# Kernel optimization log

Hardware: AMD Instinct MI355X
Metric: run time of the kernel (lower is better)

## Reference

```python
import jax, jax.numpy as jnp
import numpy as np

NUM_HEADS = 8
NUM_KV_HEADS = 2
HEAD_DIM = 64
EPS = 1e-6
ROPE_BASE = 10000.0


def rmsnorm(x, w):
    # x: (..., head_dim)
    var = jnp.mean(x * x, axis=-1, keepdims=True)
    return x * jax.lax.rsqrt(var + EPS) * w


def apply_rope(x):
    # x: (B, L, nH, hd); positions along L, standard rotate-half RoPE
    B, L, nH, hd = x.shape
    inv_freq = 1.0 / (ROPE_BASE ** (jnp.arange(0, hd, 2, dtype=jnp.float32) / hd))  # (hd/2,)
    ang = jnp.arange(L, dtype=jnp.float32)[:, None] * inv_freq[None, :]  # (L, hd/2)
    cos = jnp.concatenate([jnp.cos(ang), jnp.cos(ang)], axis=-1)[None, :, None, :]  # (1,L,1,hd)
    sin = jnp.concatenate([jnp.sin(ang), jnp.sin(ang)], axis=-1)[None, :, None, :]
    x1, x2 = jnp.split(x, 2, axis=-1)
    rot = jnp.concatenate([-x2, x1], axis=-1)
    return x * cos + rot * sin


def setup_inputs() -> dict:
    key = jax.random.key(0)
    ks = jax.random.split(key, 6)
    width = 512
    x = jax.random.normal(ks[0], (1, 16, 16, 16, width), dtype=jnp.float32)
    s = 1.0 / np.sqrt(width)
    Wq = jax.random.normal(ks[1], (width, width), dtype=jnp.float32) * s
    Wk = jax.random.normal(ks[2], (NUM_KV_HEADS * HEAD_DIM, width), dtype=jnp.float32) * s
    Wv = jax.random.normal(ks[3], (NUM_KV_HEADS * HEAD_DIM, width), dtype=jnp.float32) * s
    Wo = jax.random.normal(ks[4], (width, width), dtype=jnp.float32) * s
    q_norm_w = jnp.ones((HEAD_DIM,), dtype=jnp.float32)
    k_norm_w = jnp.ones((HEAD_DIM,), dtype=jnp.float32)
    return {"x": x, "Wq": Wq, "Wk": Wk, "Wv": Wv,
            "q_norm_w": q_norm_w, "k_norm_w": k_norm_w, "Wo": Wo}


def reference(x, Wq, Wk, Wv, q_norm_w, k_norm_w, Wo):
    B, H, W, D, C = x.shape
    L = H * W * D
    xf = x.reshape(B, L, C)
    q = (xf @ Wq.T).reshape(B, L, NUM_HEADS, HEAD_DIM)
    k = (xf @ Wk.T).reshape(B, L, NUM_KV_HEADS, HEAD_DIM)
    v = (xf @ Wv.T).reshape(B, L, NUM_KV_HEADS, HEAD_DIM)
    q = apply_rope(rmsnorm(q, q_norm_w))
    k = apply_rope(rmsnorm(k, k_norm_w))
    # (B, heads, L, hd)
    q = q.transpose(0, 2, 1, 3)
    k = k.transpose(0, 2, 1, 3)
    v = v.transpose(0, 2, 1, 3)
    repeats = NUM_HEADS // NUM_KV_HEADS
    if repeats > 1:
        k = jnp.repeat(k, repeats, axis=1)
        v = jnp.repeat(v, repeats, axis=1)
    scale = 1.0 / np.sqrt(HEAD_DIM)
    scores = jnp.einsum('bhqd,bhkd->bhqk', q, k) * scale
    attn = jax.nn.softmax(scores, axis=-1)
    out = jnp.einsum('bhqk,bhkd->bhqd', attn, v)
    out = out.transpose(0, 2, 1, 3).reshape(B, H, W, D, C)
    return out @ Wo.T
```

## Files before the change

### kernel.cpp

```cpp
#include <hip/hip_runtime.h>
#include <hip/hip_bf16.h>
#include <math.h>

#define L_SEQ 4096
#define CDIM  512
#define NH    8
#define NKV   2
#define HD    64
#define EPS   1e-6f
#define QSCALE 0.18033688011f

using short8 = __attribute__((ext_vector_type(8))) short;
using f32x4  = __attribute__((ext_vector_type(4))) float;
using f32x16 = __attribute__((ext_vector_type(16))) float;
typedef unsigned short ushort_t;

__device__ __forceinline__ ushort_t f2bf(float f) {
    union { float f; unsigned u; } c; c.f = f;
    unsigned r = c.u + 0x7FFF + ((c.u >> 16) & 1);
    return (ushort_t)(r >> 16);
}
__device__ __forceinline__ float bf2f(ushort_t u) {
    union { unsigned u; float f; } c; c.u = ((unsigned)u) << 16;
    return c.f;
}

#define GLOAD_LDS16(g, l)                                                  \
    __builtin_amdgcn_global_load_lds(                                      \
        (const __attribute__((address_space(1))) unsigned int*)(g),        \
        (__attribute__((address_space(3))) unsigned int*)(l), 16, 0, 0)

__device__ __forceinline__ short8 lds_read8(const char* p) {
    return *reinterpret_cast<const short8*>(__builtin_assume_aligned(p, 16));
}

__device__ __forceinline__ unsigned pk_bf16(float lo, float hi) {
    const __hip_bfloat162 h2 = __float22bfloat162_rn(make_float2(lo, hi));
    unsigned w; __builtin_memcpy(&w, &h2, 4);
    return w;
}

__global__ __launch_bounds__(256) void cvt_bf16(const float* __restrict__ x,
                                                const float* __restrict__ wq,
                                                const float* __restrict__ wk,
                                                const float* __restrict__ wv,
                                                const float* __restrict__ wo,
                                                ushort_t* __restrict__ xb,
                                                ushort_t* __restrict__ wqb,
                                                ushort_t* __restrict__ wkb,
                                                ushort_t* __restrict__ wvb,
                                                ushort_t* __restrict__ wob) {
    const size_t i = ((size_t)blockIdx.x * 256 + threadIdx.x) << 2;
    const float* s; ushort_t* d; size_t o;
    if (i < 2097152)      { s = x;  d = xb;  o = i; }
    else if (i < 2359296) { s = wq; d = wqb; o = i - 2097152; }
    else if (i < 2424832) { s = wk; d = wkb; o = i - 2359296; }
    else if (i < 2490368) { s = wv; d = wvb; o = i - 2424832; }
    else                  { s = wo; d = wob; o = i - 2490368; }
    const float4 v = *reinterpret_cast<const float4*>(s + o);
    ushort_t r[4] = { f2bf(v.x), f2bf(v.y), f2bf(v.z), f2bf(v.w) };
    *reinterpret_cast<uint2*>(d + o) = *reinterpret_cast<const uint2*>(r);
}

template<bool OUT_BF16>
__global__ __launch_bounds__(256) void gemm_bf16_nt(const ushort_t* __restrict__ A,
                                                    const ushort_t* __restrict__ B,
                                                    void* __restrict__ Cv,
                                                    int M, int N, int K) {
    __shared__ short As[2][4096];
    __shared__ short Bs[2][4096];

    const int tid = threadIdx.x;
    const int w = tid >> 6, lane = tid & 63;
    const int g = lane >> 4, r16 = lane & 15;
    const int wr = w >> 1, wc = w & 1;
    const int m0 = blockIdx.y * 64, n0 = blockIdx.x * 64;
    const int r7sw = (r16 & 7) << 4;

    const int lrow = lane >> 3;
    const int swzb = ((lane & 7) ^ lrow) << 4;
    const int c0 = w * 2, c1 = w * 2 + 1;
    const size_t rowK2 = (size_t)K * 2;

    const char* agA = (const char*)A + (size_t)(m0 + c0 * 8 + lrow) * rowK2 + swzb;
    const char* agB = agA + 8 * rowK2;
    const char* bgA = (const char*)B + (size_t)(n0 + c0 * 8 + lrow) * rowK2 + swzb;
    const char* bgB = bgA + 8 * rowK2;

    GLOAD_LDS16(agA, (char*)As[0] + c0 * 1024);
    GLOAD_LDS16(agB, (char*)As[0] + c1 * 1024);
    GLOAD_LDS16(bgA, (char*)Bs[0] + c0 * 1024);
    GLOAD_LDS16(bgB, (char*)Bs[0] + c1 * 1024);
    __syncthreads();

    f32x4 acc[2][2] = {};
    const int NKIT = K >> 6;
    int cur = 0;
    for (int it = 0; it < NKIT; ++it) {
        if (it + 1 < NKIT) {
            const size_t ko = (size_t)(it + 1) * 128;
            char* ad = (char*)As[cur ^ 1];
            char* bd = (char*)Bs[cur ^ 1];
            GLOAD_LDS16(agA + ko, ad + c0 * 1024);
            GLOAD_LDS16(agB + ko, ad + c1 * 1024);
            GLOAD_LDS16(bgA + ko, bd + c0 * 1024);
            GLOAD_LDS16(bgB + ko, bd + c1 * 1024);
        }
        const char* at = (const char*)As[cur];
        const char* bt = (const char*)Bs[cur];

        short8 af[2][2], bfr[2][2];
#pragma unroll
        for (int t = 0; t < 2; ++t)
#pragma unroll
            for (int ks = 0; ks < 2; ++ks) {
                af[t][ks]  = lds_read8(at + (wr * 32 + t * 16 + r16) * 128
                                          + ((ks * 64 + g * 16) ^ r7sw));
                bfr[t][ks] = lds_read8(bt + (wc * 32 + t * 16 + r16) * 128
                                          + ((ks * 64 + g * 16) ^ r7sw));
            }
        __builtin_amdgcn_s_setprio(1);
#pragma unroll
        for (int tm = 0; tm < 2; ++tm)
#pragma unroll
            for (int tn = 0; tn < 2; ++tn)
#pragma unroll
                for (int ks = 0; ks < 2; ++ks)
                    acc[tm][tn] = __builtin_amdgcn_mfma_f32_16x16x32_bf16(
                        af[tm][ks], bfr[tn][ks], acc[tm][tn], 0, 0, 0);
        __builtin_amdgcn_s_setprio(0);

        __syncthreads();
        cur ^= 1;
    }

#pragma unroll
    for (int tm = 0; tm < 2; ++tm)
#pragma unroll
        for (int tn = 0; tn < 2; ++tn)
#pragma unroll
            for (int jj = 0; jj < 4; ++jj) {
                const int row = m0 + wr * 32 + tm * 16 + g * 4 + jj;
                const int col = n0 + wc * 32 + tn * 16 + r16;
                if (OUT_BF16)
                    ((ushort_t*)Cv)[(size_t)row * N + col] = f2bf(acc[tm][tn][jj]);
                else
                    ((float*)Cv)[(size_t)row * N + col] = acc[tm][tn][jj];
            }
}

__global__ __launch_bounds__(256) void norm_rope(ushort_t* __restrict__ q,
                                                 ushort_t* __restrict__ k,
                                                 const float* __restrict__ qw,
                                                 const float* __restrict__ kw) {
    const int wid  = threadIdx.x >> 6;
    const int lane = threadIdx.x & 63;
    const long row = (long)blockIdx.x * 4 + wid;
    const long QROWS = (long)L_SEQ * NH;

    ushort_t* ptr;
    const float* w;
    int pos;
    const bool isq = (row < QROWS);
    if (isq) {
        pos = (int)(row >> 3);
        ptr = q + (size_t)pos * (NH * HD) + (int)(row & 7) * HD;
        w = qw;
    } else {
        const long r = row - QROWS;
        pos = (int)(r >> 1);
        ptr = k + (size_t)pos * (NKV * HD) + (int)(r & 1) * HD;
        w = kw;
    }

    float x = bf2f(ptr[lane]);
    float ss = x * x;
#pragma unroll
    for (int off = 32; off; off >>= 1) ss += __shfl_xor(ss, off);
    float xn = x * rsqrtf(ss * (1.0f / 64.0f) + EPS) * w[lane];

    float xp = __shfl_xor(xn, 32);
    const int i = lane & 31;
    const float inv_freq = exp2f((float)i * -0.41524101186f);
    float s, c;
    sincosf((float)pos * inv_freq, &s, &c);
    float out = (lane < 32) ? (xn * c - xp * s) : (xn * c + xp * s);
    if (isq) out *= QSCALE;
    ptr[lane] = f2bf(out);
}

__global__ __launch_bounds__(256, 2) void attn_mfma(const ushort_t* __restrict__ qb,
                                                    const ushort_t* __restrict__ kb,
                                                    const ushort_t* __restrict__ vtb,
                                                    ushort_t* __restrict__ opart,
                                                    float* __restrict__ lpart) {
    __shared__ short Ks[2][4096];
    __shared__ short Vs[2][4096];

    const int tid = threadIdx.x;
    const int w = tid >> 6, lane = tid & 63;
    const int l31 = lane & 31, hf = lane >> 5;
    const int h = blockIdx.y, hkv = h >> 2;
    const int s = blockIdx.z;
    const int kvspan = L_SEQ / gridDim.z;
    const int kvb = s * kvspan;
    const int qw = blockIdx.x * 256 + w * 64;
    const int swz = (lane & 7) << 4;

    const int lrow = lane >> 3;
    const int swzb = ((lane & 7) ^ lrow) << 4;
    const int c0 = w * 2, c1 = w * 2 + 1;

    const char* kgA = (const char*)kb + (size_t)(kvb + c0 * 8 + lrow) * (NKV * HD * 2)
                      + hkv * (HD * 2) + swzb;
    const char* kgB = kgA + 8 * (NKV * HD * 2);
    const char* vgA = (const char*)vtb + (size_t)(hkv * HD + c0 * 8 + lrow) * (L_SEQ * 2)
                      + (size_t)kvb * 2 + swzb;
    const char* vgB = vgA + 8 * (size_t)(L_SEQ * 2);

    short8 qf0[4], qf1[4];
#pragma unroll
    for (int ks = 0; ks < 4; ++ks) {
        qf0[ks] = *reinterpret_cast<const short8*>(
            &qb[(size_t)(qw + l31) * CDIM + h * HD + ks * 16 + hf * 8]);
        qf1[ks] = *reinterpret_cast<const short8*>(
            &qb[(size_t)(qw + 32 + l31) * CDIM + h * HD + ks * 16 + hf * 8]);
    }

    GLOAD_LDS16(kgA, (char*)Ks[0] + c0 * 1024);
    GLOAD_LDS16(kgB, (char*)Ks[0] + c1 * 1024);
    GLOAD_LDS16(vgA, (char*)Vs[0] + c0 * 1024);
    GLOAD_LDS16(vgB, (char*)Vs[0] + c1 * 1024);
    __syncthreads();

    f32x16 oacc0[2] = {}, oacc1[2] = {};
    float ls0[2] = {}, ls1[2] = {};

    int cur = 0;
    const int nit = kvspan >> 6;
    for (int it = 0; it < nit; ++it) {
        if (it + 1 < nit) {
            const size_t ko = (size_t)(it + 1) * 64 * (NKV * HD * 2);
            const size_t vo = (size_t)(it + 1) * 128;
            char* kd = (char*)Ks[cur ^ 1];
            char* vd = (char*)Vs[cur ^ 1];
            GLOAD_LDS16(kgA + ko, kd + c0 * 1024);
            GLOAD_LDS16(kgB + ko, kd + c1 * 1024);
            GLOAD_LDS16(vgA + vo, vd + c0 * 1024);
            GLOAD_LDS16(vgB + vo, vd + c1 * 1024);
        }

        const char* kt = (const char*)Ks[cur];
        const char* vt = (const char*)Vs[cur];

#pragma unroll
        for (int sub = 0; sub < 2; ++sub) {
            f32x16 s0 = {}, s1 = {};
            __builtin_amdgcn_s_setprio(1);
#pragma unroll
            for (int ks = 0; ks < 4; ++ks) {
                const short8 kfr = lds_read8(
                    kt + (sub * 32 + l31) * 128 + ((ks * 32 + hf * 16) ^ swz));
                s0 = __builtin_amdgcn_mfma_f32_32x32x16_bf16(kfr, qf0[ks], s0, 0, 0, 0);
                s1 = __builtin_amdgcn_mfma_f32_32x32x16_bf16(kfr, qf1[ks], s1, 0, 0, 0);
            }
            __builtin_amdgcn_s_setprio(0);

            unsigned pk0[8], pk1[8];
#pragma unroll
            for (int r2 = 0; r2 < 8; ++r2) {
                const float x0 = exp2f(s0[2 * r2]), y0 = exp2f(s0[2 * r2 + 1]);
                const float x1 = exp2f(s1[2 * r2]), y1 = exp2f(s1[2 * r2 + 1]);
                ls0[r2 & 1] += x0 + y0;
                ls1[r2 & 1] += x1 + y1;
                pk0[r2] = pk_bf16(x0, y0);
                pk1[r2] = pk_bf16(x1, y1);
            }

            short8 pf0[2], pf1[2];
#pragma unroll
            for (int kkl = 0; kkl < 2; ++kkl) {
                auto a0 = __builtin_amdgcn_permlane32_swap(pk0[kkl * 4 + 0], pk0[kkl * 4 + 2], false, false);
                auto a1 = __builtin_amdgcn_permlane32_swap(pk0[kkl * 4 + 1], pk0[kkl * 4 + 3], false, false);
                auto b0 = __builtin_amdgcn_permlane32_swap(pk1[kkl * 4 + 0], pk1[kkl * 4 + 2], false, false);
                auto b1 = __builtin_amdgcn_permlane32_swap(pk1[kkl * 4 + 1], pk1[kkl * 4 + 3], false, false);
                union { unsigned u[4]; short8 s8; } u0, u1;
                u0.u[0] = a0[0]; u0.u[1] = a1[0]; u0.u[2] = a0[1]; u0.u[3] = a1[1];
                u1.u[0] = b0[0]; u1.u[1] = b1[0]; u1.u[2] = b0[1]; u1.u[3] = b1[1];
                pf0[kkl] = u0.s8; pf1[kkl] = u1.s8;
            }

            __builtin_amdgcn_s_setprio(1);
#pragma unroll
            for (int n = 0; n < 2; ++n) {
#pragma unroll
                for (int kkl = 0; kkl < 2; ++kkl) {
                    const short8 vf = lds_read8(
                        vt + (n * 32 + l31) * 128 + (((sub * 2 + kkl) * 32 + hf * 16) ^ swz));
                    oacc0[n] = __builtin_amdgcn_mfma_f32_32x32x16_bf16(pf0[kkl], vf, oacc0[n], 0, 0, 0);
                    oacc1[n] = __builtin_amdgcn_mfma_f32_32x32x16_bf16(pf1[kkl], vf, oacc1[n], 0, 0, 0);
                }
            }
            __builtin_amdgcn_s_setprio(0);
        }

        __syncthreads();
        cur ^= 1;
    }

    float lsA = ls0[0] + ls0[1];
    float lsB = ls1[0] + ls1[1];
    lsA += __shfl_xor(lsA, 32);
    lsB += __shfl_xor(lsB, 32);
    ushort_t* op = opart + (size_t)s * L_SEQ * CDIM;
    float* lp = lpart + (size_t)s * L_SEQ * NH;
    if (lane < 32) {
        lp[(size_t)(qw + lane) * NH + h] = lsA;
        lp[(size_t)(qw + 32 + lane) * NH + h] = lsB;
    }
#pragma unroll
    for (int n = 0; n < 2; ++n)
#pragma unroll
        for (int r = 0; r < 16; ++r) {
            const int rr = (r & 3) + 8 * (r >> 2) + 4 * hf;
            op[(size_t)(qw + rr) * CDIM + h * HD + n * 32 + l31] = f2bf(oacc0[n][r]);
            op[(size_t)(qw + 32 + rr) * CDIM + h * HD + n * 32 + l31] = f2bf(oacc1[n][r]);
        }
}

__global__ __launch_bounds__(256) void combine_splits(const ushort_t* __restrict__ opart,
                                                      const float* __restrict__ lpart,
                                                      ushort_t* __restrict__ out,
                                                      int nsplit) {
    const size_t i4 = ((size_t)blockIdx.x * 256 + threadIdx.x) << 2;
    const int row = (int)(i4 >> 9);
    const int h = (int)((i4 & 511) >> 6);
    float l = 0.0f;
    for (int s = 0; s < nsplit; ++s)
        l += lpart[(size_t)s * L_SEQ * NH + (size_t)row * NH + h];
    const float inv = 1.0f / l;

    float acc[4] = {};
    for (int s = 0; s < nsplit; ++s) {
        ushort_t a[4];
        *reinterpret_cast<uint2*>(a) =
            *reinterpret_cast<const uint2*>(opart + (size_t)s * L_SEQ * CDIM + i4);
#pragma unroll
        for (int j = 0; j < 4; ++j) acc[j] += bf2f(a[j]);
    }
    ushort_t r[4];
#pragma unroll
    for (int j = 0; j < 4; ++j) r[j] = f2bf(acc[j] * inv);
    *reinterpret_cast<uint2*>(out + i4) = *reinterpret_cast<const uint2*>(r);
}

extern "C" void kernel_launch(void* const* d_in, const int* in_sizes, int n_in,
                              void* d_out, int out_size, void* d_ws, size_t ws_size,
                              hipStream_t stream) {
    const float* x   = (const float*)d_in[0];
    const float* Wq  = (const float*)d_in[1];
    const float* Wk  = (const float*)d_in[2];
    const float* Wv  = (const float*)d_in[3];
    const float* qnw = (const float*)d_in[4];
    const float* knw = (const float*)d_in[5];
    const float* Wo  = (const float*)d_in[6];
    float* out = (float*)d_out;

    const size_t tail = (size_t)L_SEQ * CDIM * 2
                      + (size_t)L_SEQ * NKV * HD * 2 * 2
                      + (size_t)CDIM * CDIM * 2 * 2
                      + (size_t)NKV * HD * CDIM * 2 * 2
                      + (size_t)8 * L_SEQ * NH * 4;
    const size_t need8 = (size_t)8 * L_SEQ * CDIM * 2 + tail;
    const int nsplit = (ws_size >= need8) ? 8 : 4;

    char* p = (char*)d_ws;
    ushort_t* opart = (ushort_t*)p;
    ushort_t* xb    = opart;
    ushort_t* abuf  = opart;
    char* q = p + (size_t)nsplit * L_SEQ * CDIM * 2;
    ushort_t* qbuf = (ushort_t*)q;
    ushort_t* kbuf = qbuf + (size_t)L_SEQ * CDIM;
    ushort_t* vtb  = kbuf + (size_t)L_SEQ * NKV * HD;
    ushort_t* wqb  = vtb  + (size_t)L_SEQ * NKV * HD;
    ushort_t* wkb  = wqb  + (size_t)CDIM * CDIM;
    ushort_t* wvb  = wkb  + (size_t)NKV * HD * CDIM;
    ushort_t* wob  = wvb  + (size_t)NKV * HD * CDIM;
    float*    lpart = (float*)(wob + (size_t)CDIM * CDIM);

    const dim3 blk(256);

    cvt_bf16<<<dim3(2688), blk, 0, stream>>>(x, Wq, Wk, Wv, Wo, xb, wqb, wkb, wvb, wob);

    gemm_bf16_nt<true><<<dim3(8, 64),  blk, 0, stream>>>(xb, wqb, qbuf, L_SEQ, CDIM, CDIM);
    gemm_bf16_nt<true><<<dim3(2, 64),  blk, 0, stream>>>(xb, wkb, kbuf, L_SEQ, NKV * HD, CDIM);
    gemm_bf16_nt<true><<<dim3(64, 2),  blk, 0, stream>>>(wvb, xb, vtb, NKV * HD, L_SEQ, CDIM);

    norm_rope<<<dim3((L_SEQ * (NH + NKV)) / 4), blk, 0, stream>>>(qbuf, kbuf, qnw, knw);

    attn_mfma<<<dim3(L_SEQ / 256, NH, nsplit), blk, 0, stream>>>(qbuf, kbuf, vtb, opart, lpart);

    combine_splits<<<dim3((L_SEQ * CDIM) / (256 * 4)), blk, 0, stream>>>(opart, lpart, abuf, nsplit);

    gemm_bf16_nt<false><<<dim3(8, 64), blk, 0, stream>>>(abuf, wob, out, L_SEQ, CDIM, CDIM);
}
```

Measured before the change: 115.1 us.

## Fuse Q/K/V projections and RMSNorm+RoPE into one GEMM kernel

Replaces three separate projection GEMM launches and the standalone norm_rope kernel with a single qkv_gemm kernel. Block IDs are partitioned across the Q, K and transposed V products. For Q and K tiles, the accumulator is staged through shared memory so RMSNorm, RoPE and the Q scale are applied before the bf16 store. This removes three launches and a full read-modify-write pass over Q and K in global memory, at the cost of an extra LDS staging pass and serial per-row epilogue work inside each GEMM block.

New measurement: 102.5 us. -11.0%, faster.

```diff
diff --git a/kernel.cpp b/kernel.cpp
--- a/kernel.cpp
+++ b/kernel.cpp
@@ -62,6 +62,135 @@
     *reinterpret_cast<uint2*>(d + o) = *reinterpret_cast<const uint2*>(r);
 }
 
+__global__ __launch_bounds__(256) void qkv_gemm(const ushort_t* __restrict__ xb,
+                                                const ushort_t* __restrict__ wqb,
+                                                const ushort_t* __restrict__ wkb,
+                                                const ushort_t* __restrict__ wvb,
+                                                const float* __restrict__ qnw,
+                                                const float* __restrict__ knw,
+                                                ushort_t* __restrict__ qbuf,
+                                                ushort_t* __restrict__ kbuf,
+                                                ushort_t* __restrict__ vtb) {
+    __shared__ char smem[32768];
+    short (*As)[4096] = (short(*)[4096])smem;
+    short (*Bs)[4096] = (short(*)[4096])(smem + 16384);
+    float (*F)[65]    = (float(*)[65])smem;
+
+    const int bid = blockIdx.x;
+    int which, m0, n0;
+    const ushort_t *A, *B;
+    if (bid < 512)      { which = 0; A = xb;  B = wqb; m0 = (bid >> 3) * 64; n0 = (bid & 7) * 64; }
+    else if (bid < 640) { which = 1; A = xb;  B = wkb; const int i = bid - 512; m0 = (i >> 1) * 64; n0 = (i & 1) * 64; }
+    else                { which = 2; A = wvb; B = xb;  const int i = bid - 640; m0 = (i & 1) * 64; n0 = (i >> 1) * 64; }
+
+    const int tid = threadIdx.x;
+    const int w = tid >> 6, lane = tid & 63;
+    const int g = lane >> 4, r16 = lane & 15;
+    const int wr = w >> 1, wc = w & 1;
+    const int r7sw = (r16 & 7) << 4;
+
+    const int lrow = lane >> 3;
+    const int swzb = ((lane & 7) ^ lrow) << 4;
+    const int c0 = w * 2, c1 = w * 2 + 1;
+    const size_t rowK2 = (size_t)CDIM * 2;
+
+    const char* agA = (const char*)A + (size_t)(m0 + c0 * 8 + lrow) * rowK2 + swzb;
+    const char* agB = agA + 8 * rowK2;
+    const char* bgA = (const char*)B + (size_t)(n0 + c0 * 8 + lrow) * rowK2 + swzb;
+    const char* bgB = bgA + 8 * rowK2;
+
+    GLOAD_LDS16(agA, (char*)As[0] + c0 * 1024);
+    GLOAD_LDS16(agB, (char*)As[0] + c1 * 1024);
+    GLOAD_LDS16(bgA, (char*)Bs[0] + c0 * 1024);
+    GLOAD_LDS16(bgB, (char*)Bs[0] + c1 * 1024);
+    __syncthreads();
+
+    f32x4 acc[2][2] = {};
+    int cur = 0;
+    for (int it = 0; it < CDIM / 64; ++it) {
+        if (it + 1 < CDIM / 64) {
+            const size_t ko = (size_t)(it + 1) * 128;
+            char* ad = (char*)As[cur ^ 1];
+            char* bd = (char*)Bs[cur ^ 1];
+            GLOAD_LDS16(agA + ko, ad + c0 * 1024);
+            GLOAD_LDS16(agB + ko, ad + c1 * 1024);
+            GLOAD_LDS16(bgA + ko, bd + c0 * 1024);
+            GLOAD_LDS16(bgB + ko, bd + c1 * 1024);
+        }
+        const char* at = (const char*)As[cur];
+        const char* bt = (const char*)Bs[cur];
+
+        short8 af[2][2], bfr[2][2];
+#pragma unroll
+        for (int t = 0; t < 2; ++t)
+#pragma unroll
+            for (int ks = 0; ks < 2; ++ks) {
+                af[t][ks]  = lds_read8(at + (wr * 32 + t * 16 + r16) * 128
+                                          + ((ks * 64 + g * 16) ^ r7sw));
+                bfr[t][ks] = lds_read8(bt + (wc * 32 + t * 16 + r16) * 128
+                                          + ((ks * 64 + g * 16) ^ r7sw));
+            }
+        __builtin_amdgcn_s_setprio(1);
+#pragma unroll
+        for (int tm = 0; tm < 2; ++tm)
+#pragma unroll
+            for (int tn = 0; tn < 2; ++tn)
+#pragma unroll
+                for (int ks = 0; ks < 2; ++ks)
+                    acc[tm][tn] = __builtin_amdgcn_mfma_f32_16x16x32_bf16(
+                        af[tm][ks], bfr[tn][ks], acc[tm][tn], 0, 0, 0);
+        __builtin_amdgcn_s_setprio(0);
+
+        __syncthreads();
+        cur ^= 1;
+    }
+
+    if (which == 2) {
+#pragma unroll
+        for (int tm = 0; tm < 2; ++tm)
+#pragma unroll
+            for (int tn = 0; tn < 2; ++tn)
+#pragma unroll
+                for (int jj = 0; jj < 4; ++jj) {
+                    const int row = m0 + wr * 32 + tm * 16 + g * 4 + jj;
+                    const int col = n0 + wc * 32 + tn * 16 + r16;
+                    vtb[(size_t)row * L_SEQ + col] = f2bf(acc[tm][tn][jj]);
+                }
+        return;
+    }
+
+#pragma unroll
+    for (int tm = 0; tm < 2; ++tm)
+#pragma unroll
+        for (int tn = 0; tn < 2; ++tn)
+#pragma unroll
+            for (int jj = 0; jj < 4; ++jj)
+                F[wr * 32 + tm * 16 + g * 4 + jj][wc * 32 + tn * 16 + r16] = acc[tm][tn][jj];
+    __syncthreads();
+
+    const float wv_ = (which == 0 ? qnw : knw)[lane];
+    const int i31 = lane & 31;
+    const float invf = exp2f((float)i31 * -0.41524101186f);
+    ushort_t* dst = (which == 0) ? qbuf : kbuf;
+    const int ncols = (which == 0) ? (NH * HD) : (NKV * HD);
+
+    for (int rr = 0; rr < 16; ++rr) {
+        const int rl = w * 16 + rr;
+        const int pos = m0 + rl;
+        float x = F[rl][lane];
+        float ss = x * x;
+#pragma unroll
+        for (int off = 32; off; off >>= 1) ss += __shfl_xor(ss, off);
+        float xn = x * rsqrtf(ss * (1.0f / 64.0f) + EPS) * wv_;
+        float xp = __shfl_xor(xn, 32);
+        float sn, cs;
+        sincosf((float)pos * invf, &sn, &cs);
+        float out = (lane < 32) ? (xn * cs - xp * sn) : (xn * cs + xp * sn);
+        if (which == 0) out *= QSCALE;
+        dst[(size_t)pos * ncols + n0 + lane] = f2bf(out);
+    }
+}
+
 template<bool OUT_BF16>
 __global__ __launch_bounds__(256) void gemm_bf16_nt(const ushort_t* __restrict__ A,
                                                     const ushort_t* __restrict__ B,
@@ -149,46 +278,6 @@
             }
 }
 
-__global__ __launch_bounds__(256) void norm_rope(ushort_t* __restrict__ q,
-                                                 ushort_t* __restrict__ k,
-                                                 const float* __restrict__ qw,
-                                                 const float* __restrict__ kw) {
-    const int wid  = threadIdx.x >> 6;
-    const int lane = threadIdx.x & 63;
-    const long row = (long)blockIdx.x * 4 + wid;
-    const long QROWS = (long)L_SEQ * NH;
-
-    ushort_t* ptr;
-    const float* w;
-    int pos;
-    const bool isq = (row < QROWS);
-    if (isq) {
-        pos = (int)(row >> 3);
-        ptr = q + (size_t)pos * (NH * HD) + (int)(row & 7) * HD;
-        w = qw;
-    } else {
-        const long r = row - QROWS;
-        pos = (int)(r >> 1);
-        ptr = k + (size_t)pos * (NKV * HD) + (int)(r & 1) * HD;
-        w = kw;
-    }
-
-    float x = bf2f(ptr[lane]);
-    float ss = x * x;
-#pragma unroll
-    for (int off = 32; off; off >>= 1) ss += __shfl_xor(ss, off);
-    float xn = x * rsqrtf(ss * (1.0f / 64.0f) + EPS) * w[lane];
-
-    float xp = __shfl_xor(xn, 32);
-    const int i = lane & 31;
-    const float inv_freq = exp2f((float)i * -0.41524101186f);
-    float s, c;
-    sincosf((float)pos * inv_freq, &s, &c);
-    float out = (lane < 32) ? (xn * c - xp * s) : (xn * c + xp * s);
-    if (isq) out *= QSCALE;
-    ptr[lane] = f2bf(out);
-}
-
 __global__ __launch_bounds__(256, 2) void attn_mfma(const ushort_t* __restrict__ qb,
                                                     const ushort_t* __restrict__ kb,
                                                     const ushort_t* __restrict__ vtb,
@@ -392,11 +481,7 @@
 
     cvt_bf16<<<dim3(2688), blk, 0, stream>>>(x, Wq, Wk, Wv, Wo, xb, wqb, wkb, wvb, wob);
 
-    gemm_bf16_nt<true><<<dim3(8, 64),  blk, 0, stream>>>(xb, wqb, qbuf, L_SEQ, CDIM, CDIM);
-    gemm_bf16_nt<true><<<dim3(2, 64),  blk, 0, stream>>>(xb, wkb, kbuf, L_SEQ, NKV * HD, CDIM);
-    gemm_bf16_nt<true><<<dim3(64, 2),  blk, 0, stream>>>(wvb, xb, vtb, NKV * HD, L_SEQ, CDIM);
-
-    norm_rope<<<dim3((L_SEQ * (NH + NKV)) / 4), blk, 0, stream>>>(qbuf, kbuf, qnw, knw);
+    qkv_gemm<<<dim3(768), blk, 0, stream>>>(xb, wqb, wkb, wvb, qnw, knw, qbuf, kbuf, vtb);
 
     attn_mfma<<<dim3(L_SEQ / 256, NH, nsplit), blk, 0, stream>>>(qbuf, kbuf, vtb, opart, lpart);
 
```

## Merge Q/K/V projections into one 128-tile GEMM with fused norm+RoPE epilogue

Applied to the files above, without the earlier changes.

Replaces the three separate 64x64-tile projection GEMMs and the standalone norm_rope kernel with a single 128x128-tile kernel. It dispatches Q, K and V^T tiles by block index and applies RMSNorm and RoPE in an LDS-staged epilogue. The output projection also moves to 128x128 tiles, and the attention split count is fixed at 4 instead of being picked from workspace size. This removes three launches and one round trip of Q/K through global memory and raises per-block MFMA reuse. The cost is fewer blocks (192 for QKV, 128 for Wo), which may underfill the GPU, and the forced split of 4 may lower attention parallelism.

Measured after the change: 117.0 us. Within noise of the previous version (+1.6%).

```diff
diff --git a/kernel.cpp b/kernel.cpp
--- a/kernel.cpp
+++ b/kernel.cpp
@@ -9,6 +9,7 @@
 #define HD    64
 #define EPS   1e-6f
 #define QSCALE 0.18033688011f
+#define NSPLIT 4
 
 using short8 = __attribute__((ext_vector_type(8))) short;
 using f32x4  = __attribute__((ext_vector_type(4))) float;
@@ -62,131 +63,158 @@
     *reinterpret_cast<uint2*>(d + o) = *reinterpret_cast<const uint2*>(r);
 }
 
-template<bool OUT_BF16>
-__global__ __launch_bounds__(256) void gemm_bf16_nt(const ushort_t* __restrict__ A,
-                                                    const ushort_t* __restrict__ B,
-                                                    void* __restrict__ Cv,
-                                                    int M, int N, int K) {
-    __shared__ short As[2][4096];
-    __shared__ short Bs[2][4096];
-
-    const int tid = threadIdx.x;
-    const int w = tid >> 6, lane = tid & 63;
-    const int g = lane >> 4, r16 = lane & 15;
-    const int wr = w >> 1, wc = w & 1;
-    const int m0 = blockIdx.y * 64, n0 = blockIdx.x * 64;
-    const int r7sw = (r16 & 7) << 4;
-
-    const int lrow = lane >> 3;
-    const int swzb = ((lane & 7) ^ lrow) << 4;
-    const int c0 = w * 2, c1 = w * 2 + 1;
-    const size_t rowK2 = (size_t)K * 2;
-
-    const char* agA = (const char*)A + (size_t)(m0 + c0 * 8 + lrow) * rowK2 + swzb;
-    const char* agB = agA + 8 * rowK2;
-    const char* bgA = (const char*)B + (size_t)(n0 + c0 * 8 + lrow) * rowK2 + swzb;
-    const char* bgB = bgA + 8 * rowK2;
-
-    GLOAD_LDS16(agA, (char*)As[0] + c0 * 1024);
-    GLOAD_LDS16(agB, (char*)As[0] + c1 * 1024);
-    GLOAD_LDS16(bgA, (char*)Bs[0] + c0 * 1024);
-    GLOAD_LDS16(bgB, (char*)Bs[0] + c1 * 1024);
+#define GEMM128_CORE(A_, B_, K_)                                              \
+    const int tid = threadIdx.x;                                              \
+    const int w = tid >> 6, lane = tid & 63;                                  \
+    const int g = lane >> 4, r16 = lane & 15;                                 \
+    const int wr = w >> 1, wc = w & 1;                                        \
+    const int r7sw = (r16 & 7) << 4;                                          \
+    const int lrow = lane >> 3;                                               \
+    const int swzb = ((lane & 7) ^ lrow) << 4;                                \
+    char* As[2] = { smem, smem + 16384 };                                     \
+    char* Bs[2] = { smem + 32768, smem + 49152 };                             \
+    const size_t rowK2 = (size_t)(K_) * 2;                                    \
+    const char* ag[4]; const char* bg[4];                                     \
+    _Pragma("unroll")                                                         \
+    for (int c = 0; c < 4; ++c) {                                             \
+        const int ch = w * 4 + c;                                             \
+        ag[c] = (const char*)(A_) + (size_t)(m0 + ch * 8 + lrow) * rowK2 + swzb; \
+        bg[c] = (const char*)(B_) + (size_t)(n0 + ch * 8 + lrow) * rowK2 + swzb; \
+    }                                                                         \
+    _Pragma("unroll")                                                         \
+    for (int c = 0; c < 4; ++c) {                                             \
+        GLOAD_LDS16(ag[c], As[0] + (w * 4 + c) * 1024);                       \
+        GLOAD_LDS16(bg[c], Bs[0] + (w * 4 + c) * 1024);                       \
+    }                                                                         \
+    __syncthreads();                                                          \
+    f32x4 acc[4][4] = {};                                                     \
+    const int NKIT = (K_) >> 6;                                               \
+    int cur = 0;                                                              \
+    for (int it = 0; it < NKIT; ++it) {                                       \
+        if (it + 1 < NKIT) {                                                  \
+            const size_t ko = (size_t)(it + 1) * 128;                         \
+            _Pragma("unroll")                                                 \
+            for (int c = 0; c < 4; ++c) {                                     \
+                GLOAD_LDS16(ag[c] + ko, As[cur ^ 1] + (w * 4 + c) * 1024);    \
+                GLOAD_LDS16(bg[c] + ko, Bs[cur ^ 1] + (w * 4 + c) * 1024);    \
+            }                                                                 \
+        }                                                                     \
+        const char* at = As[cur];                                             \
+        const char* bt = Bs[cur];                                             \
+        short8 af[4][2], bf[4][2];                                            \
+        _Pragma("unroll")                                                     \
+        for (int t = 0; t < 4; ++t)                                           \
+            _Pragma("unroll")                                                 \
+            for (int ks = 0; ks < 2; ++ks) {                                  \
+                af[t][ks] = lds_read8(at + (wr * 64 + t * 16 + r16) * 128     \
+                                         + ((ks * 64 + g * 16) ^ r7sw));      \
+                bf[t][ks] = lds_read8(bt + (wc * 64 + t * 16 + r16) * 128     \
+                                         + ((ks * 64 + g * 16) ^ r7sw));      \
+            }                                                                 \
+        __builtin_amdgcn_s_setprio(1);                                        \
+        _Pragma("unroll")                                                     \
+        for (int tm = 0; tm < 4; ++tm)                                        \
+            _Pragma("unroll")                                                 \
+            for (int tn = 0; tn < 4; ++tn)                                    \
+                _Pragma("unroll")                                             \
+                for (int ks = 0; ks < 2; ++ks)                                \
+                    acc[tm][tn] = __builtin_amdgcn_mfma_f32_16x16x32_bf16(    \
+                        af[tm][ks], bf[tn][ks], acc[tm][tn], 0, 0, 0);        \
+        __builtin_amdgcn_s_setprio(0);                                        \
+        __syncthreads();                                                      \
+        cur ^= 1;                                                             \
+    }
+
+__global__ __launch_bounds__(256, 2) void qkv_gemm128(const ushort_t* __restrict__ xb,
+                                                      const ushort_t* __restrict__ wqb,
+                                                      const ushort_t* __restrict__ wkb,
+                                                      const ushort_t* __restrict__ wvb,
+                                                      const float* __restrict__ qnw,
+                                                      const float* __restrict__ knw,
+                                                      ushort_t* __restrict__ qbuf,
+                                                      ushort_t* __restrict__ kbuf,
+                                                      ushort_t* __restrict__ vtb) {
+    __shared__ char smem[128 * 130 * 4];
+    float (*F)[130] = (float(*)[130])smem;
+
+    const int bid = blockIdx.x;
+    int which, m0, n0;
+    const ushort_t *A, *B;
+    if (bid < 128)      { which = 0; A = xb;  B = wqb; m0 = (bid >> 2) * 128; n0 = (bid & 3) * 128; }
+    else if (bid < 160) { which = 1; A = xb;  B = wkb; m0 = (bid - 128) * 128; n0 = 0; }
+    else                { which = 2; A = wvb; B = xb;  m0 = 0; n0 = (bid - 160) * 128; }
+
+    GEMM128_CORE(A, B, CDIM)
+
+    if (which == 2) {
+#pragma unroll
+        for (int tm = 0; tm < 4; ++tm)
+#pragma unroll
+            for (int tn = 0; tn < 4; ++tn)
+#pragma unroll
+                for (int jj = 0; jj < 4; ++jj) {
+                    const int row = m0 + wr * 64 + tm * 16 + g * 4 + jj;
+                    const int col = n0 + wc * 64 + tn * 16 + r16;
+                    vtb[(size_t)row * L_SEQ + col] = f2bf(acc[tm][tn][jj]);
+                }
+        return;
+    }
+
+#pragma unroll
+    for (int tm = 0; tm < 4; ++tm)
+#pragma unroll
+        for (int tn = 0; tn < 4; ++tn)
+#pragma unroll
+            for (int jj = 0; jj < 4; ++jj)
+                F[wr * 64 + tm * 16 + g * 4 + jj][wc * 64 + tn * 16 + r16] = acc[tm][tn][jj];
     __syncthreads();
 
-    f32x4 acc[2][2] = {};
-    const int NKIT = K >> 6;
-    int cur = 0;
-    for (int it = 0; it < NKIT; ++it) {
-        if (it + 1 < NKIT) {
-            const size_t ko = (size_t)(it + 1) * 128;
-            char* ad = (char*)As[cur ^ 1];
-            char* bd = (char*)Bs[cur ^ 1];
-            GLOAD_LDS16(agA + ko, ad + c0 * 1024);
-            GLOAD_LDS16(agB + ko, ad + c1 * 1024);
-            GLOAD_LDS16(bgA + ko, bd + c0 * 1024);
-            GLOAD_LDS16(bgB + ko, bd + c1 * 1024);
+    const float wq_ = qnw[lane], wk_ = knw[lane];
+    const int i31 = lane & 31;
+    const float invf = exp2f((float)i31 * -0.41524101186f);
+
+    for (int v = 0; v < 64; ++v) {
+        const int vecid = w + 4 * v;
+        const int rl = vecid >> 1;
+        const int hh = vecid & 1;
+        const int pos = m0 + rl;
+        float x = F[rl][hh * 64 + lane];
+        float ss = x * x;
+#pragma unroll
+        for (int off = 32; off; off >>= 1) ss += __shfl_xor(ss, off);
+        const float wv_ = (which == 0) ? wq_ : wk_;
+        float xn = x * rsqrtf(ss * (1.0f / 64.0f) + EPS) * wv_;
+        float xp = __shfl_xor(xn, 32);
+        float sn, cs;
+        sincosf((float)pos * invf, &sn, &cs);
+        float out = (lane < 32) ? (xn * cs - xp * sn) : (xn * cs + xp * sn);
+        if (which == 0) {
+            out *= QSCALE;
+            qbuf[(size_t)pos * (NH * HD) + n0 + hh * 64 + lane] = f2bf(out);
+        } else {
+            kbuf[(size_t)pos * (NKV * HD) + hh * 64 + lane] = f2bf(out);
         }
-        const char* at = (const char*)As[cur];
-        const char* bt = (const char*)Bs[cur];
-
-        short8 af[2][2], bfr[2][2];
-#pragma unroll
-        for (int t = 0; t < 2; ++t)
-#pragma unroll
-            for (int ks = 0; ks < 2; ++ks) {
-                af[t][ks]  = lds_read8(at + (wr * 32 + t * 16 + r16) * 128
-                                          + ((ks * 64 + g * 16) ^ r7sw));
-                bfr[t][ks] = lds_read8(bt + (wc * 32 + t * 16 + r16) * 128
-                                          + ((ks * 64 + g * 16) ^ r7sw));
+    }
+}
+
+__global__ __launch_bounds__(256, 2) void gemm128_wo(const ushort_t* __restrict__ A_,
+                                                     const ushort_t* __restrict__ B_,
+                                                     float* __restrict__ C) {
+    __shared__ char smem[65536];
+    const int m0 = blockIdx.y * 128, n0 = blockIdx.x * 128;
+
+    GEMM128_CORE(A_, B_, CDIM)
+
+#pragma unroll
+    for (int tm = 0; tm < 4; ++tm)
+#pragma unroll
+        for (int tn = 0; tn < 4; ++tn)
+#pragma unroll
+            for (int jj = 0; jj < 4; ++jj) {
+                const int row = m0 + wr * 64 + tm * 16 + g * 4 + jj;
+                const int col = n0 + wc * 64 + tn * 16 + r16;
+                C[(size_t)row * CDIM + col] = acc[tm][tn][jj];
             }
-        __builtin_amdgcn_s_setprio(1);
-#pragma unroll
-        for (int tm = 0; tm < 2; ++tm)
-#pragma unroll
-            for (int tn = 0; tn < 2; ++tn)
-#pragma unroll
-                for (int ks = 0; ks < 2; ++ks)
-                    acc[tm][tn] = __builtin_amdgcn_mfma_f32_16x16x32_bf16(
-                        af[tm][ks], bfr[tn][ks], acc[tm][tn], 0, 0, 0);
-        __builtin_amdgcn_s_setprio(0);
-
-        __syncthreads();
-        cur ^= 1;
-    }
-
-#pragma unroll
-    for (int tm = 0; tm < 2; ++tm)
-#pragma unroll
-        for (int tn = 0; tn < 2; ++tn)
-#pragma unroll
-            for (int jj = 0; jj < 4; ++jj) {
-                const int row = m0 + wr * 32 + tm * 16 + g * 4 + jj;
-                const int col = n0 + wc * 32 + tn * 16 + r16;
-                if (OUT_BF16)
-                    ((ushort_t*)Cv)[(size_t)row * N + col] = f2bf(acc[tm][tn][jj]);
-                else
-                    ((float*)Cv)[(size_t)row * N + col] = acc[tm][tn][jj];
-            }
-}
-
-__global__ __launch_bounds__(256) void norm_rope(ushort_t* __restrict__ q,
-                                                 ushort_t* __restrict__ k,
-                                                 const float* __restrict__ qw,
-                                                 const float* __restrict__ kw) {
-    const int wid  = threadIdx.x >> 6;
-    const int lane = threadIdx.x & 63;
-    const long row = (long)blockIdx.x * 4 + wid;
-    const long QROWS = (long)L_SEQ * NH;
-
-    ushort_t* ptr;
-    const float* w;
-    int pos;
-    const bool isq = (row < QROWS);
-    if (isq) {
-        pos = (int)(row >> 3);
-        ptr = q + (size_t)pos * (NH * HD) + (int)(row & 7) * HD;
-        w = qw;
-    } else {
-        const long r = row - QROWS;
-        pos = (int)(r >> 1);
-        ptr = k + (size_t)pos * (NKV * HD) + (int)(r & 1) * HD;
-        w = kw;
-    }
-
-    float x = bf2f(ptr[lane]);
-    float ss = x * x;
-#pragma unroll
-    for (int off = 32; off; off >>= 1) ss += __shfl_xor(ss, off);
-    float xn = x * rsqrtf(ss * (1.0f / 64.0f) + EPS) * w[lane];
-
-    float xp = __shfl_xor(xn, 32);
-    const int i = lane & 31;
-    const float inv_freq = exp2f((float)i * -0.41524101186f);
-    float s, c;
-    sincosf((float)pos * inv_freq, &s, &c);
-    float out = (lane < 32) ? (xn * c - xp * s) : (xn * c + xp * s);
-    if (isq) out *= QSCALE;
-    ptr[lane] = f2bf(out);
 }
 
 __global__ __launch_bounds__(256, 2) void attn_mfma(const ushort_t* __restrict__ qb,
@@ -366,19 +394,11 @@
     const float* Wo  = (const float*)d_in[6];
     float* out = (float*)d_out;
 
-    const size_t tail = (size_t)L_SEQ * CDIM * 2
-                      + (size_t)L_SEQ * NKV * HD * 2 * 2
-                      + (size_t)CDIM * CDIM * 2 * 2
-                      + (size_t)NKV * HD * CDIM * 2 * 2
-                      + (size_t)8 * L_SEQ * NH * 4;
-    const size_t need8 = (size_t)8 * L_SEQ * CDIM * 2 + tail;
-    const int nsplit = (ws_size >= need8) ? 8 : 4;
-
     char* p = (char*)d_ws;
     ushort_t* opart = (ushort_t*)p;
     ushort_t* xb    = opart;
     ushort_t* abuf  = opart;
-    char* q = p + (size_t)nsplit * L_SEQ * CDIM * 2;
+    char* q = p + (size_t)NSPLIT * L_SEQ * CDIM * 2;
     ushort_t* qbuf = (ushort_t*)q;
     ushort_t* kbuf = qbuf + (size_t)L_SEQ * CDIM;
     ushort_t* vtb  = kbuf + (size_t)L_SEQ * NKV * HD;
@@ -392,15 +412,11 @@
 
     cvt_bf16<<<dim3(2688), blk, 0, stream>>>(x, Wq, Wk, Wv, Wo, xb, wqb, wkb, wvb, wob);
 
-    gemm_bf16_nt<true><<<dim3(8, 64),  blk, 0, stream>>>(xb, wqb, qbuf, L_SEQ, CDIM, CDIM);
-    gemm_bf16_nt<true><<<dim3(2, 64),  blk, 0, stream>>>(xb, wkb, kbuf, L_SEQ, NKV * HD, CDIM);
-    gemm_bf16_nt<true><<<dim3(64, 2),  blk, 0, stream>>>(wvb, xb, vtb, NKV * HD, L_SEQ, CDIM);
-
-    norm_rope<<<dim3((L_SEQ * (NH + NKV)) / 4), blk, 0, stream>>>(qbuf, kbuf, qnw, knw);
-
-    attn_mfma<<<dim3(L_SEQ / 256, NH, nsplit), blk, 0, stream>>>(qbuf, kbuf, vtb, opart, lpart);
-
-    combine_splits<<<dim3((L_SEQ * CDIM) / (256 * 4)), blk, 0, stream>>>(opart, lpart, abuf, nsplit);
-
-    gemm_bf16_nt<false><<<dim3(8, 64), blk, 0, stream>>>(abuf, wob, out, L_SEQ, CDIM, CDIM);
-}
+    qkv_gemm128<<<dim3(192), blk, 0, stream>>>(xb, wqb, wkb, wvb, qnw, knw, qbuf, kbuf, vtb);
+
+    attn_mfma<<<dim3(L_SEQ / 256, NH, NSPLIT), blk, 0, stream>>>(qbuf, kbuf, vtb, opart, lpart);
+
+    combine_splits<<<dim3((L_SEQ * CDIM) / (256 * 4)), blk, 0, stream>>>(opart, lpart, abuf, NSPLIT);
+
+    gemm128_wo<<<dim3(CDIM / 128, L_SEQ / 128), blk, 0, stream>>>(abuf, wob, out);
+}
```
